# Kernel optimization log

Hardware: AMD Instinct MI355X
Metric: run time of the kernel (lower is better)

## Reference

```python
import jax, jax.numpy as jnp
import numpy as np

N = 4096; E = 32768; H = 128; R = 32; L = 2
CUT_UP = 5.0; MAX_Z = 100

def cosine_cutoff(d):
    c = 0.5 * (jnp.cos(d * (np.pi / CUT_UP)) + 1.0)
    return c * (d < CUT_UP).astype(d.dtype)

def tensor_norm(t):
    return (t * t).sum((-2, -1))

def decompose_tensor(t):
    eye = jnp.eye(3, dtype=t.dtype)
    I = (jnp.trace(t, axis1=-2, axis2=-1) / 3.0)[..., None, None] * eye
    tT = jnp.swapaxes(t, -2, -1)
    A = 0.5 * (t - tT)
    S = 0.5 * (t + tT) - I
    return I, A, S

def vector_to_skewtensor(v):
    x, y, z = v[..., 0], v[..., 1], v[..., 2]
    o = jnp.zeros_like(x)
    return jnp.stack([o, -z, y, z, o, -x, -y, x, o], axis=-1).reshape(v.shape[:-1] + (3, 3))

def vector_to_symtensor(v):
    t = v[..., :, None] * v[..., None, :]
    eye = jnp.eye(3, dtype=v.dtype)
    I = (jnp.trace(t, axis1=-2, axis2=-1) / 3.0)[..., None, None] * eye
    return t - I  # symmetric already, 0.5*(t+t^T) == t

def cmix(T, W):  # nn.Linear(H,H,bias=False) over the channel dim of [N,H,3,3]
    return jnp.einsum('nhij,hk->nkij', T, W)

def layernorm(x, g, b, eps=1e-5):
    m = x.mean(-1, keepdims=True)
    v = ((x - m) ** 2).mean(-1, keepdims=True)
    return (x - m) / jnp.sqrt(v + eps) * g + b

def setup_inputs():
    key = jax.random.key(0)
    ks = iter(jax.random.split(key, 48))
    def nrm(shape, fan_in):
        return jax.random.normal(next(ks), shape, jnp.float32) / np.sqrt(fan_in)
    inp = {}
    inp['z'] = jax.random.randint(next(ks), (N,), 0, MAX_Z)
    inp['edge_index'] = jax.random.randint(next(ks), (2, E), 0, N)
    inp['edge_weight'] = jax.random.uniform(next(ks), (E,), jnp.float32) * CUT_UP
    inp['edge_vec'] = jax.random.normal(next(ks), (E, 3), jnp.float32)
    inp['edge_attr'] = jax.random.normal(next(ks), (E, R), jnp.float32)
    inp['emb_table'] = nrm((MAX_Z, H), H)
    inp['dp1_w'] = nrm((R, H), R); inp['dp1_b'] = jnp.zeros((H,))
    inp['dp2_w'] = nrm((R, H), R); inp['dp2_b'] = jnp.zeros((H,))
    inp['dp3_w'] = nrm((R, H), R); inp['dp3_b'] = jnp.zeros((H,))
    inp['emb2_w'] = nrm((2 * H, H), 2 * H); inp['emb2_b'] = jnp.zeros((H,))
    inp['tne_lt'] = nrm((3, H, H), H)
    inp['tne_s0_w'] = nrm((H, 2 * H), H); inp['tne_s0_b'] = jnp.zeros((2 * H,))
    inp['tne_s1_w'] = nrm((2 * H, 3 * H), 2 * H); inp['tne_s1_b'] = jnp.zeros((3 * H,))
    inp['ln_g'] = jnp.ones((H,)); inp['ln_b'] = jnp.zeros((H,))
    inp['msg_l0_w'] = nrm((L, R, H), R); inp['msg_l0_b'] = jnp.zeros((L, H))
    inp['msg_l1_w'] = nrm((L, H, 2 * H), H); inp['msg_l1_b'] = jnp.zeros((L, 2 * H))
    inp['msg_l2_w'] = nrm((L, 2 * H, 3 * H), 2 * H); inp['msg_l2_b'] = jnp.zeros((L, 3 * H))
    inp['msg_lx'] = nrm((L, 3, H, H), H)
    inp['msg_lt'] = nrm((L, 3, H, H), H)
    return inp

def _forward(z, edge_index, edge_weight, edge_vec, edge_attr, emb_table,
             dp1_w, dp1_b, dp2_w, dp2_b, dp3_w, dp3_b, emb2_w, emb2_b,
             tne_lt, tne_s0_w, tne_s0_b, tne_s1_w, tne_s1_b, ln_g, ln_b,
             msg_l0_w, msg_l0_b, msg_l1_w, msg_l1_b, msg_l2_w, msg_l2_b,
             msg_lx, msg_lt):
    src, dst = edge_index[0], edge_index[1]
    eye = jnp.eye(3, dtype=jnp.float32)
    segsum = lambda x: jax.ops.segment_sum(x, dst, num_segments=N)
    silu = jax.nn.silu
    # ---- TensorNeighborEmbedding ----
    Z = emb_table[z]                                     # [N,H]
    C = cosine_cutoff(edge_weight)                       # [E]
    W1 = (edge_attr @ dp1_w + dp1_b) * C[:, None]
    W2 = (edge_attr @ dp2_w + dp2_b) * C[:, None]
    W3 = (edge_attr @ dp3_w + dp3_b) * C[:, None]
    mask = (src != dst)[:, None]
    vn = jnp.linalg.norm(edge_vec, axis=-1, keepdims=True)
    ev = jnp.where(mask, edge_vec / jnp.maximum(vn, 1e-12), edge_vec)
    skew = vector_to_skewtensor(ev)                      # [E,3,3]
    sym = vector_to_symtensor(ev)                        # [E,3,3]
    Zij = jnp.concatenate([Z[dst], Z[src]], axis=-1) @ emb2_w + emb2_b  # [E,H]
    # I channel is a scaled identity per edge -> factor the eye out of the scatter
    In = segsum(Zij * W1)[..., None, None] * eye                         # [N,H,3,3]
    An = segsum((Zij * W2)[:, :, None, None] * skew[:, None])            # [N,H,3,3]
    Sn = segsum((Zij * W3)[:, :, None, None] * sym[:, None])             # [N,H,3,3]
    norm = layernorm(tensor_norm(In + An + Sn), ln_g, ln_b)              # [N,H]
    In = cmix(In, tne_lt[0]); An = cmix(An, tne_lt[1]); Sn = cmix(Sn, tne_lt[2])
    fsc = silu(silu(norm @ tne_s0_w + tne_s0_b) @ tne_s1_w + tne_s1_b).reshape(N, H, 3)
    X = (fsc[..., 0, None, None] * In + fsc[..., 1, None, None] * An
         + fsc[..., 2, None, None] * Sn)
    # ---- TensorMessage layers ----
    for l in range(L):
        ea = silu(edge_attr @ msg_l0_w[l] + msg_l0_b[l])
        ea = silu(ea @ msg_l1_w[l] + msg_l1_b[l])
        ea = silu(ea @ msg_l2_w[l] + msg_l2_b[l])
        ea = (ea * C[:, None]).reshape(E, H, 3)
        X = X / (tensor_norm(X) + 1.0)[..., None, None]
        I, A, S = decompose_tensor(X)
        I = cmix(I, msg_lx[l, 0]); A = cmix(A, msg_lx[l, 1]); S = cmix(S, msg_lx[l, 2])
        Y = I + A + S
        Im = segsum(ea[:, :, 0, None, None] * I[src])    # gather -> scale -> scatter
        Am = segsum(ea[:, :, 1, None, None] * A[src])
        Sm = segsum(ea[:, :, 2, None, None] * S[src])
        msg = Im + Am + Sm
        AB = msg @ Y + Y @ msg                           # batched 3x3 matmuls
        I, A, S = decompose_tensor(AB)
        d = (tensor_norm(I + A + S) + 1.0)[..., None, None]
        I = cmix(I / d, msg_lt[l, 0]); A = cmix(A / d, msg_lt[l, 1]); S = cmix(S / d, msg_lt[l, 2])
        dX = I + A + S
        dX = dX + dX @ dX
        X = X + dX
    return X

def reference(z, edge_index, edge_weight, edge_vec, edge_attr, emb_table,
              dp1_w, dp1_b, dp2_w, dp2_b, dp3_w, dp3_b, emb2_w, emb2_b,
              tne_lt, tne_s0_w, tne_s0_b, tne_s1_w, tne_s1_b, ln_g, ln_b,
              msg_l0_w, msg_l0_b, msg_l1_w, msg_l1_b, msg_l2_w, msg_l2_b,
              msg_lx, msg_lt):
    return _forward(z, edge_index, edge_weight, edge_vec, edge_attr, emb_table,
                    dp1_w, dp1_b, dp2_w, dp2_b, dp3_w, dp3_b, emb2_w, emb2_b,
                    tne_lt, tne_s0_w, tne_s0_b, tne_s1_w, tne_s1_b, ln_g, ln_b,
                    msg_l0_w, msg_l0_b, msg_l1_w, msg_l1_b, msg_l2_w, msg_l2_b,
                    msg_lx, msg_lt)
```

## Files before the change

### kernel.cpp

```cpp
#include <hip/hip_runtime.h>
#include <hip/hip_bf16.h>

typedef __hip_bfloat16 bf16;
typedef __attribute__((ext_vector_type(8))) short short8v;
typedef __attribute__((ext_vector_type(4))) float f32x4;

#define NN 4096
#define NE 32768
#define HH 128
#define MAXZ 100
#define TPB 8
#define NB 2


__device__ __forceinline__ float b2f(bf16 v){ return __bfloat162float(v); }
__device__ __forceinline__ float ldf(const float* p, size_t i){ return p[i]; }
__device__ __forceinline__ float ldf(const bf16*  p, size_t i){ return __bfloat162float(p[i]); }
__device__ __forceinline__ float siluf(float x){ return x / (1.0f + __expf(-x)); }
__device__ __forceinline__ unsigned short f2bu(float x){
  bf16 h = __float2bfloat16(x);
  return *reinterpret_cast<unsigned short*>(&h);
}

__global__ void __launch_bounds__(256) k_detect(const unsigned int* __restrict__ w, int* __restrict__ flag){
  __shared__ int cnt[256];
  int t = threadIdx.x;
  int c = 0;
  for (int i = t; i < 4096; i += 256){
    unsigned int lo = w[i] & 0xffffu;
    int e = (int)((lo >> 7) & 0xffu);
    c += (e >= 110 && e <= 132) ? 1 : 0;
  }
  cnt[t] = c; __syncthreads();
  for (int off=128; off>=1; off>>=1){ if (t<off) cnt[t]+=cnt[t+off]; __syncthreads(); }
  if (t==0) flag[0] = (cnt[0] < 2048) ? 1 : 0;
}

__global__ void __launch_bounds__(256) k_count(const int* __restrict__ dst, int* __restrict__ counts){
  int e = blockIdx.x*256 + threadIdx.x;
  if (e < NE) atomicAdd(&counts[dst[e]], 1);
}

__global__ void __launch_bounds__(1024) k_scan(const int* __restrict__ counts, int* __restrict__ offsets, int* __restrict__ cursor){
  __shared__ int lds[1024];
  int t = threadIdx.x;
  int c0 = counts[4*t+0], c1 = counts[4*t+1], c2 = counts[4*t+2], c3 = counts[4*t+3];
  int s1 = c0+c1, s2 = s1+c2, s3 = s2+c3;
  lds[t] = s3;
  __syncthreads();
  for (int off=1; off<1024; off<<=1){
    int v = lds[t];
    int add = (t>=off)? lds[t-off] : 0;
    __syncthreads();
    lds[t] = v + add;
    __syncthreads();
  }
  int incl = lds[t];
  int base = incl - s3;
  offsets[4*t+0]=base;    offsets[4*t+1]=base+c0; offsets[4*t+2]=base+s1; offsets[4*t+3]=base+s2;
  cursor [4*t+0]=base;    cursor [4*t+1]=base+c0; cursor [4*t+2]=base+s1; cursor [4*t+3]=base+s2;
  if (t==1023) offsets[4096]=incl;
}

__global__ void __launch_bounds__(256) k_fill(const int* __restrict__ dst, const int* __restrict__ src,
                                              int* __restrict__ cursor,
                                              int* __restrict__ pos, int* __restrict__ csrc){
  int e = blockIdx.x*256 + threadIdx.x;
  if (e < NE){
    int p = atomicAdd(&cursor[dst[e]], 1);
    pos[e] = p;
    csrc[p] = src[e];
  }
}

template<typename T>
__device__ __forceinline__ void geom_impl(const T* ew, const T* evec,
    const int* src, const int* dst, const int* pos, float* gC, float* gVp){
  int e = blockIdx.x*256 + threadIdx.x;
  if (e >= NE) return;
  float d = ldf(ew, e);
  float c = 0.5f*(cosf(d*0.6283185307179586f)+1.0f);
  c = (d < 5.0f) ? c : 0.0f;
  gC[e] = c;
  float x = ldf(evec, (size_t)e*3+0), y = ldf(evec, (size_t)e*3+1), z = ldf(evec, (size_t)e*3+2);
  if (src[e] != dst[e]){
    float n = sqrtf(x*x+y*y+z*z);
    float inv = 1.0f/fmaxf(n, 1e-12f);
    x*=inv; y*=inv; z*=inv;
  }
  int p = pos[e];
  gVp[p*3+0]=x; gVp[p*3+1]=y; gVp[p*3+2]=z;
}
__global__ void __launch_bounds__(256) k_geom(const void* ew, const void* evec,
    const int* __restrict__ src, const int* __restrict__ dst, const int* __restrict__ pos,
    float* __restrict__ gC, float* __restrict__ gVp, const int* __restrict__ flag){
  if (flag[0]) geom_impl<float>((const float*)ew, (const float*)evec, src, dst, pos, gC, gVp);
  else         geom_impl<bf16 >((const bf16* )ew, (const bf16* )evec, src, dst, pos, gC, gVp);
}

template<typename T>
__device__ __forceinline__ void zemb_impl(const T* emb, const T* emb2_w,
    float* P1z, float* P2z, float* Zr){
  int zv = blockIdx.x, h = threadIdx.x;
  Zr[h] = ldf(emb, (size_t)zv*HH + h);
// ... 210 lines not shown
  for (int ks=0; ks<8; ++ks) a3[ks] = *reinterpret_cast<const short8v*>(&h2p[ks*512 + lane*8]);
  for (int nt=wid; nt<24; nt+=4){
    float bias = ldf(b1, nt*16+m);
    f32x4 acc = {bias,bias,bias,bias};
    #pragma unroll
    for (int ks=0; ks<8; ++ks){
      short8v b = *reinterpret_cast<const short8v*>(ps1 + ((size_t)(nt*8+ks)*64 + lane)*8);
      acc = __builtin_amdgcn_mfma_f32_16x16x32_bf16(a3[ks], b, acc, 0,0,0);
    }
    #pragma unroll
    for (int r=0;r<4;++r){
      int n = nt*16 + m, row = g*4 + r;
      ((unsigned short*)fsc3)[(size_t)(n0+row)*384 + (n%3)*128 + (n/3)] = f2bu(siluf(acc[r]));
    }
  }
}
__global__ void __launch_bounds__(256) k_node_mlp(
  const bf16* __restrict__ lnO, const unsigned short* __restrict__ ps0,
  const unsigned short* __restrict__ ps1,
  const void* b0, const void* b1, bf16* __restrict__ fsc3, const int* __restrict__ flag)
{
  __shared__ __align__(16) unsigned short h2p[4096];
  if (flag[0]) node_mlp_impl<float>(lnO, ps0, ps1, (const float*)b0, (const float*)b1, fsc3, h2p);
  else         node_mlp_impl<bf16 >(lnO, ps0, ps1, (const bf16* )b0, (const bf16* )b1, fsc3, h2p);
}

__global__ void __launch_bounds__(256) k_tne_cmix(
  const bf16* __restrict__ sm10, const unsigned short* __restrict__ pwlt,
  const bf16* __restrict__ fsc3, float* __restrict__ X9)
{
  int wid  = threadIdx.x >> 6;
  int lane = threadIdx.x & 63;
  int n0 = blockIdx.x*16;
  int m = lane & 15, g = lane >> 4;
  f32x4 acc[10][2];
  #pragma unroll
  for (int c=0;c<10;++c){ acc[c][0]=(f32x4){0,0,0,0}; acc[c][1]=(f32x4){0,0,0,0}; }
  #pragma unroll
  for (int c=0;c<10;++c){
    int mat = (c==0) ? 0 : (c<4) ? 1 : 2;
    const unsigned short* bw = pwlt + (size_t)mat*16384;
    short8v af[4];
    #pragma unroll
    for (int ks=0; ks<4; ++ks)
      af[ks] = *reinterpret_cast<const short8v*>((const unsigned short*)sm10 + (size_t)(n0+m)*1280 + c*128 + ks*32 + g*8);
    #pragma unroll
    for (int t=0;t<2;++t){
      int nt = wid + t*4;
      #pragma unroll
      for (int ks=0; ks<4; ++ks){
        short8v b = *reinterpret_cast<const short8v*>(bw + ((size_t)(nt*4+ks)*64 + lane)*8);
        acc[c][t] = __builtin_amdgcn_mfma_f32_16x16x32_bf16(af[ks], b, acc[c][t], 0,0,0);
      }
    }
  }
  #pragma unroll
  for (int t=0;t<2;++t){
    int nt = wid + t*4;
    int h = nt*16 + m;
    #pragma unroll
    for (int r=0;r<4;++r){
      int node = n0 + g*4 + r;
      float am  = acc[0][t][r];
      float wm0 = acc[1][t][r], wm1 = acc[2][t][r], wm2 = acc[3][t][r];
      float t0 = acc[4][t][r], t1 = acc[5][t][r], t2 = acc[6][t][r];
      float t3 = acc[7][t][r], t4 = acc[8][t][r], t5 = acc[9][t][r];
      float f0 = b2f(fsc3[(size_t)node*384 + h]);
      float f1 = b2f(fsc3[(size_t)node*384 + 128 + h]);
      float f2 = b2f(fsc3[(size_t)node*384 + 256 + h]);
      float* xp = X9 + (size_t)node*1152;
      xp[0*128+h] = f0*am + f2*t0;
      xp[1*128+h] = -f1*wm2 + f2*t1;
      xp[2*128+h] =  f1*wm1 + f2*t2;
      xp[3*128+h] =  f1*wm2 + f2*t1;
      xp[4*128+h] = f0*am + f2*t3;
      xp[5*128+h] = -f1*wm0 + f2*t4;
      xp[6*128+h] = -f1*wm1 + f2*t2;
      xp[7*128+h] =  f1*wm0 + f2*t4;
      xp[8*128+h] = f0*am + f2*t5;
    }
  }
}

__global__ void __launch_bounds__(256) k_cmix10(
  const bf16* __restrict__ in10, const unsigned short* __restrict__ pw,
  bf16* __restrict__ out10)
{
  int wid  = threadIdx.x >> 6;
  int lane = threadIdx.x & 63;
  int n0 = blockIdx.x*16;
  int m = lane & 15, g = lane >> 4;
  f32x4 acc[10][2];
  #pragma unroll
  for (int c=0;c<10;++c){ acc[c][0]=(f32x4){0,0,0,0}; acc[c][1]=(f32x4){0,0,0,0}; }
  #pragma unroll
  for (int c=0;c<10;++c){
    int mat = (c==0) ? 0 : (c<4) ? 1 : 2;
    const unsigned short* bw = pw + (size_t)mat*16384;
    short8v af[4];
    #pragma unroll
    for (int ks=0; ks<4; ++ks)
      af[ks] = *reinterpret_cast<const short8v*>((const unsigned short*)in10 + (size_t)(n0+m)*1280 + c*128 + ks*32 + g*8);
    #pragma unroll
    for (int t=0;t<2;++t){
      int nt = wid + t*4;
      #pragma unroll
      for (int ks=0; ks<4; ++ks){
        short8v b = *reinterpret_cast<const short8v*>(bw + ((size_t)(nt*4+ks)*64 + lane)*8);
        acc[c][t] = __builtin_amdgcn_mfma_f32_16x16x32_bf16(af[ks], b, acc[c][t], 0,0,0);
      }
    }
  }
  __syncthreads();
  #pragma unroll
  for (int t=0;t<2;++t){
    int nt = wid + t*4;
    int h = nt*16 + m;
    #pragma unroll
    for (int r=0;r<4;++r){
      int node = n0 + g*4 + r;
      unsigned short* op = (unsigned short*)out10 + (size_t)node*1280;
      #pragma unroll
      for (int c=0;c<10;++c) op[c*128 + h] = f2bu(acc[c][t][r]);
    }
  }
}

template<typename T>
__device__ __forceinline__ void mfma_impl(
  const unsigned short* eattr_c, const float* gC, const int* pos,
  const unsigned short* p0, const unsigned short* p1, const unsigned short* p2,
  const T* b0, const T* b1, const T* b2,
  unsigned short* eabuf, unsigned short (*h1p)[2048], unsigned short (*h2p)[4096], int* spos)
{
  int wid  = threadIdx.x >> 6;
  int lane = threadIdx.x & 63;
  int e0 = blockIdx.x*32;
  int m = lane & 15, g = lane >> 4;
  if (threadIdx.x < 32) spos[threadIdx.x] = pos[e0 + threadIdx.x];
  float cc[2][4];
  #pragma unroll
  for (int mt=0;mt<2;++mt)
    #pragma unroll
    for (int r=0;r<4;++r) cc[mt][r] = gC[e0 + mt*16 + g*4 + r];
  short8v a1[2];
  #pragma unroll
  for (int mt=0;mt<2;++mt)
    a1[mt] = *reinterpret_cast<const short8v*>(eattr_c + (size_t)(e0+mt*16+m)*32 + g*8);
  for (int nt=wid; nt<8; nt+=4){
    float bias = ldf(b0, nt*16+m);
    short8v b = *reinterpret_cast<const short8v*>(p0 + ((size_t)nt*64 + lane)*8);
    #pragma unroll
    for (int mt=0;mt<2;++mt){
      f32x4 acc = {bias,bias,bias,bias};
      acc = __builtin_amdgcn_mfma_f32_16x16x32_bf16(a1[mt], b, acc, 0,0,0);
      #pragma unroll
      for (int r=0;r<4;++r){
        int n = nt*16 + m, row = g*4 + r;
        h1p[mt][(n>>5)*512 + (((n>>3)&3)*16+row)*8 + (n&7)] = f2bu(siluf(acc[r]));
      }
    }
  }
  __syncthreads();
  short8v a2[2][4];
  #pragma unroll
  for (int mt=0;mt<2;++mt)
    #pragma unroll
    for (int ks=0; ks<4; ++ks)
      a2[mt][ks] = *reinterpret_cast<const short8v*>(&h1p[mt][ks*512 + lane*8]);
  for (int nt=wid; nt<16; nt+=4){
    float bias = ldf(b1, nt*16+m);
    short8v bfr[4];
    #pragma unroll
    for (int ks=0; ks<4; ++ks)
      bfr[ks] = *reinterpret_cast<const short8v*>(p1 + ((size_t)(nt*4+ks)*64 + lane)*8);
    #pragma unroll
    for (int mt=0;mt<2;++mt){
      f32x4 acc = {bias,bias,bias,bias};
      #pragma unroll
      for (int ks=0; ks<4; ++ks)
        acc = __builtin_amdgcn_mfma_f32_16x16x32_bf16(a2[mt][ks], bfr[ks], acc, 0,0,0);
      #pragma unroll
      for (int r=0;r<4;++r){
        int n = nt*16 + m, row = g*4 + r;
        h2p[mt][(n>>5)*512 + (((n>>3)&3)*16+row)*8 + (n&7)] = f2bu(siluf(acc[r]));
      }
    }
  }
  __syncthreads();
  short8v a3[2][8];
  #pragma unroll
  for (int mt=0;mt<2;++mt)
    #pragma unroll
    for (int ks=0; ks<8; ++ks)
      a3[mt][ks] = *reinterpret_cast<const short8v*>(&h2p[mt][ks*512 + lane*8]);
  for (int nt=wid; nt<24; nt+=4){
    float bias = ldf(b2, nt*16+m);
    short8v bfr[8];
    #pragma unroll
    for (int ks=0; ks<8; ++ks)
      bfr[ks] = *reinterpret_cast<const short8v*>(p2 + ((size_t)(nt*8+ks)*64 + lane)*8);
    #pragma unroll
    for (int mt=0;mt<2;++mt){
      f32x4 acc = {bias,bias,bias,bias};
      #pragma unroll
      for (int ks=0; ks<8; ++ks)
        acc = __builtin_amdgcn_mfma_f32_16x16x32_bf16(a3[mt][ks], bfr[ks], acc, 0,0,0);
      #pragma unroll
      for (int r=0;r<4;++r){
        int n = nt*16 + m, row = g*4 + r;
        float v = siluf(acc[r]) * cc[mt][r];
        eabuf[(size_t)spos[mt*16+row]*384 + (n%3)*128 + (n/3)] = f2bu(v);
      }
    }
  }
}
__global__ void __launch_bounds__(256) k_msg_edge_mfma(
  const unsigned short* __restrict__ eattr_c, const float* __restrict__ gC,
  const int* __restrict__ pos,
  const unsigned short* __restrict__ p0, const unsigned short* __restrict__ p1,
  const unsigned short* __restrict__ p2,
  const void* b0, const void* b1, const void* b2, long boff0, long boff1, long boff2,
  unsigned short* __restrict__ eabuf, const int* __restrict__ flag)
{
  __shared__ __align__(16) unsigned short h1p[2][2048];
  __shared__ __align__(16) unsigned short h2p[2][4096];
  __shared__ int spos[32];
  if (flag[0]) mfma_impl<float>(eattr_c, gC, pos, p0, p1, p2,
      (const float*)b0 + boff0, (const float*)b1 + boff1, (const float*)b2 + boff2, eabuf, h1p, h2p, spos);
  else mfma_impl<bf16>(eattr_c, gC, pos, p0, p1, p2,
      (const bf16*)b0 + boff0, (const bf16*)b1 + boff1, (const bf16*)b2 + boff2, eabuf, h1p, h2p, spos);
}

__global__ void __launch_bounds__(128) k_msg_norm(
  float* __restrict__ X9, bf16* __restrict__ smb)
{
  int n0 = blockIdx.x*NB, h = threadIdx.x;
  #pragma unroll
  for (int nn=0;nn<NB;++nn){
    int n = n0+nn;
    float* xp = X9 + (size_t)n*1152;
    float x00=xp[0*128+h], x01=xp[1*128+h], x02=xp[2*128+h];
    float x10=xp[3*128+h], x11=xp[4*128+h], x12=xp[5*128+h];
    float x20=xp[6*128+h], x21=xp[7*128+h], x22=xp[8*128+h];
    float tn = x00*x00+x01*x01+x02*x02+x10*x10+x11*x11+x12*x12+x20*x20+x21*x21+x22*x22;
    float inv = 1.0f/(tn+1.0f);
    x00*=inv; x01*=inv; x02*=inv; x10*=inv; x11*=inv; x12*=inv; x20*=inv; x21*=inv; x22*=inv;
    xp[0*128+h]=x00; xp[1*128+h]=x01; xp[2*128+h]=x02;
    xp[3*128+h]=x10; xp[4*128+h]=x11; xp[5*128+h]=x12;
    xp[6*128+h]=x20; xp[7*128+h]=x21; xp[8*128+h]=x22;
    float a = (x00+x11+x22)*(1.0f/3.0f);
    bf16* sp = smb + (size_t)n*1280;
    sp[0*128+h]=__float2bfloat16(a);
    sp[1*128+h]=__float2bfloat16(0.5f*(x21-x12));
    sp[2*128+h]=__float2bfloat16(0.5f*(x02-x20));
    sp[3*128+h]=__float2bfloat16(0.5f*(x10-x01));
    sp[4*128+h]=__float2bfloat16(x00-a);
    sp[5*128+h]=__float2bfloat16(0.5f*(x01+x10));
    sp[6*128+h]=__float2bfloat16(0.5f*(x02+x20));
    sp[7*128+h]=__float2bfloat16(x11-a);
    sp[8*128+h]=__float2bfloat16(0.5f*(x12+x21));
    sp[9*128+h]=__float2bfloat16(x22-a);
  }
}

__global__ void __launch_bounds__(128) k_msg_sab(
  const int* __restrict__ offsets, const int* __restrict__ csrc,
  const bf16* __restrict__ eabuf, const bf16* __restrict__ Y10, bf16* __restrict__ smb)
{
  int n0 = blockIdx.x*NB, h = threadIdx.x;
  #pragma unroll
  for (int nn=0;nn<NB;++nn){
    int n = n0+nn;
    float am=0, vm0=0,vm1=0,vm2=0, smm0=0,smm1=0,smm2=0,smm3=0,smm4=0,smm5=0;
    int beg = offsets[n], end = offsets[n+1];
    int i = beg;
    for (; i+4 <= end; i += 4){
      int ss[4];
      #pragma unroll
      for (int u=0;u<4;++u){ ss[u] = csrc[i+u]; }
      float e0a[4], e1a[4], e2a[4];
      float y0[4],y1[4],y2[4],y3[4],y4[4],y5[4],y6[4],y7[4],y8[4],y9[4];
      #pragma unroll
      for (int u=0;u<4;++u){
        const bf16* ep = eabuf + (size_t)(i+u)*384;
        e0a[u]=b2f(ep[h]); e1a[u]=b2f(ep[128+h]); e2a[u]=b2f(ep[256+h]);
        const bf16* yp = Y10 + (size_t)ss[u]*1280;
        y0[u]=b2f(yp[0*128+h]); y1[u]=b2f(yp[1*128+h]); y2[u]=b2f(yp[2*128+h]);
        y3[u]=b2f(yp[3*128+h]); y4[u]=b2f(yp[4*128+h]); y5[u]=b2f(yp[5*128+h]);
        y6[u]=b2f(yp[6*128+h]); y7[u]=b2f(yp[7*128+h]); y8[u]=b2f(yp[8*128+h]);
        y9[u]=b2f(yp[9*128+h]);
      }
      #pragma unroll
      for (int u=0;u<4;++u){
        am   += e0a[u]*y0[u];
        vm0  += e1a[u]*y1[u]; vm1 += e1a[u]*y2[u]; vm2 += e1a[u]*y3[u];
        smm0 += e2a[u]*y4[u]; smm1 += e2a[u]*y5[u]; smm2 += e2a[u]*y6[u];
        smm3 += e2a[u]*y7[u]; smm4 += e2a[u]*y8[u]; smm5 += e2a[u]*y9[u];
      }
    }
    for (; i<end; ++i){
      int s = csrc[i];
      const bf16* ep = eabuf + (size_t)i*384;
      float e0 = b2f(ep[h]), e1 = b2f(ep[128+h]), e2 = b2f(ep[256+h]);
      const bf16* yp = Y10 + (size_t)s*1280;
      am   += e0*b2f(yp[0*128+h]);
      vm0  += e1*b2f(yp[1*128+h]); vm1 += e1*b2f(yp[2*128+h]); vm2 += e1*b2f(yp[3*128+h]);
      smm0 += e2*b2f(yp[4*128+h]); smm1 += e2*b2f(yp[5*128+h]); smm2 += e2*b2f(yp[6*128+h]);
      smm3 += e2*b2f(yp[7*128+h]); smm4 += e2*b2f(yp[8*128+h]); smm5 += e2*b2f(yp[9*128+h]);
    }
    const bf16* yp = Y10 + (size_t)n*1280;
    float aY=b2f(yp[0*128+h]), u0=b2f(yp[1*128+h]), u1=b2f(yp[2*128+h]), u2=b2f(yp[3*128+h]);
    float q0=b2f(yp[4*128+h]), q1=b2f(yp[5*128+h]), q2=b2f(yp[6*128+h]);
    float q3=b2f(yp[7*128+h]), q4=b2f(yp[8*128+h]), q5=b2f(yp[9*128+h]);
    float m00=am+smm0,   m01=-vm2+smm1, m02= vm1+smm2;
    float m10= vm2+smm1, m11=am+smm3,  m12=-vm0+smm4;
    float m20=-vm1+smm2, m21= vm0+smm4, m22=am+smm5;
    float y00=aY+q0,  y01=-u2+q1, y02= u1+q2;
    float y10= u2+q1, y11=aY+q3,  y12=-u0+q4;
    float y20=-u1+q2, y21= u0+q4, y22=aY+q5;
    float ab00 = m00*y00+m01*y10+m02*y20 + y00*m00+y01*m10+y02*m20;
    float ab01 = m00*y01+m01*y11+m02*y21 + y00*m01+y01*m11+y02*m21;
    float ab02 = m00*y02+m01*y12+m02*y22 + y00*m02+y01*m12+y02*m22;
    float ab10 = m10*y00+m11*y10+m12*y20 + y10*m00+y11*m10+y12*m20;
    float ab11 = m10*y01+m11*y11+m12*y21 + y10*m01+y11*m11+y12*m21;
    float ab12 = m10*y02+m11*y12+m12*y22 + y10*m02+y11*m12+y12*m22;
    float ab20 = m20*y00+m21*y10+m22*y20 + y20*m00+y21*m10+y22*m20;
    float ab21 = m20*y01+m21*y11+m22*y21 + y20*m01+y21*m11+y22*m21;
    float ab22 = m20*y02+m21*y12+m22*y22 + y20*m02+y21*m12+y22*m22;
    float a2 = (ab00+ab11+ab22)*(1.0f/3.0f);
    float w0 = 0.5f*(ab21-ab12), w1 = 0.5f*(ab02-ab20), w2 = 0.5f*(ab10-ab01);
    float t0 = ab00-a2, t1 = 0.5f*(ab01+ab10), t2 = 0.5f*(ab02+ab20);
    float t3 = ab11-a2, t4 = 0.5f*(ab12+ab21), t5 = ab22-a2;
    float dnm = ab00*ab00+ab01*ab01+ab02*ab02+ab10*ab10+ab11*ab11+ab12*ab12
              + ab20*ab20+ab21*ab21+ab22*ab22 + 1.0f;
    float inv = 1.0f/dnm;
    bf16* sp = smb + (size_t)n*1280;
    sp[0*128+h]=__float2bfloat16(a2*inv);
    sp[1*128+h]=__float2bfloat16(w0*inv); sp[2*128+h]=__float2bfloat16(w1*inv); sp[3*128+h]=__float2bfloat16(w2*inv);
    sp[4*128+h]=__float2bfloat16(t0*inv); sp[5*128+h]=__float2bfloat16(t1*inv); sp[6*128+h]=__float2bfloat16(t2*inv);
    sp[7*128+h]=__float2bfloat16(t3*inv); sp[8*128+h]=__float2bfloat16(t4*inv); sp[9*128+h]=__float2bfloat16(t5*inv);
  }
}

template<typename T>
__device__ __forceinline__ void fin_impl(
  const bf16* smb, float* X9, T* out, int write_out)
{
  int n0 = blockIdx.x*NB, h = threadIdx.x;
  #pragma unroll
  for (int nn=0;nn<NB;++nn){
    int n = n0+nn;
    const bf16* sp = smb + (size_t)n*1280;
    float at  = b2f(sp[0*128+h]);
    float vt0 = b2f(sp[1*128+h]), vt1 = b2f(sp[2*128+h]), vt2 = b2f(sp[3*128+h]);
    float st0 = b2f(sp[4*128+h]), st1 = b2f(sp[5*128+h]), st2 = b2f(sp[6*128+h]);
    float st3 = b2f(sp[7*128+h]), st4 = b2f(sp[8*128+h]), st5 = b2f(sp[9*128+h]);
    float d00=at+st0,   d01=-vt2+st1, d02= vt1+st2;
    float d10= vt2+st1, d11=at+st3,  d12=-vt0+st4;
    float d20=-vt1+st2, d21= vt0+st4, d22=at+st5;
    float g00 = d00 + d00*d00+d01*d10+d02*d20;
    float g01 = d01 + d00*d01+d01*d11+d02*d21;
    float g02 = d02 + d00*d02+d01*d12+d02*d22;
    float g10 = d10 + d10*d00+d11*d10+d12*d20;
    float g11 = d11 + d10*d01+d11*d11+d12*d21;
    float g12 = d12 + d10*d02+d11*d12+d12*d22;
    float g20 = d20 + d20*d00+d21*d10+d22*d20;
    float g21 = d21 + d20*d01+d21*d11+d22*d21;
    float g22 = d22 + d20*d02+d21*d12+d22*d22;
    float* xp = X9 + (size_t)n*1152;
    float x00=xp[0*128+h]+g00, x01=xp[1*128+h]+g01, x02=xp[2*128+h]+g02;
    float x10=xp[3*128+h]+g10, x11=xp[4*128+h]+g11, x12=xp[5*128+h]+g12;
    float x20=xp[6*128+h]+g20, x21=xp[7*128+h]+g21, x22=xp[8*128+h]+g22;
    if (write_out){
      if (sizeof(T)==4){
        float* of = (float*)out + ((size_t)n*128 + h)*9;
        of[0]=x00; of[1]=x01; of[2]=x02; of[3]=x10; of[4]=x11; of[5]=x12; of[6]=x20; of[7]=x21; of[8]=x22;
      } else {
        bf16* ob = (bf16*)out + ((size_t)n*128 + h)*9;
        ob[0]=__float2bfloat16(x00); ob[1]=__float2bfloat16(x01); ob[2]=__float2bfloat16(x02);
        ob[3]=__float2bfloat16(x10); ob[4]=__float2bfloat16(x11); ob[5]=__float2bfloat16(x12);
        ob[6]=__float2bfloat16(x20); ob[7]=__float2bfloat16(x21); ob[8]=__float2bfloat16(x22);
      }
    } else {
      xp[0*128+h]=x00; xp[1*128+h]=x01; xp[2*128+h]=x02;
      xp[3*128+h]=x10; xp[4*128+h]=x11; xp[5*128+h]=x12;
      xp[6*128+h]=x20; xp[7*128+h]=x21; xp[8*128+h]=x22;
    }
  }
}
__global__ void __launch_bounds__(128) k_msg_fin(
  const bf16* __restrict__ smb, float* __restrict__ X9, void* __restrict__ out,
  const int* __restrict__ flag, int write_out)
{
  if (flag[0]) fin_impl<float>(smb, X9, (float*)out, write_out);
  else         fin_impl<bf16 >(smb, X9, (bf16* )out, write_out);
}

extern "C" void kernel_launch(void* const* d_in, const int* in_sizes, int n_in,
                              void* d_out, int out_size, void* d_ws, size_t ws_size,
                              hipStream_t stream)
{
  (void)in_sizes; (void)n_in; (void)out_size; (void)ws_size;
  const int* z    = (const int*)d_in[0];
  const int* eidx = (const int*)d_in[1];
  const int* src  = eidx;
  const int* dst  = eidx + NE;

  char* w = (char*)d_ws;
  int* flag    = (int*)w;   w += 64;
  int* counts  = (int*)w;   w += (size_t)NN*4;
  int* offsets = (int*)w;   w += (size_t)(NN+1)*4 + 60;
  int* cursor  = (int*)w;   w += (size_t)NN*4;
  int* pos     = (int*)w;   w += (size_t)NE*4;
  int* csrc    = (int*)w;   w += (size_t)NE*4;
  float* gC    = (float*)w; w += (size_t)NE*4;
  float* gVp   = (float*)w; w += (size_t)NE*12;
  float* P1z   = (float*)w; w += (size_t)MAXZ*HH*4;
  float* P2z   = (float*)w; w += (size_t)MAXZ*HH*4;
  bf16* eabuf  = (bf16*)w;  w += (size_t)NE*384*2;
  float* X9    = (float*)w; w += (size_t)NN*1152*4;
  bf16* Y10    = (bf16*)w;  w += (size_t)NN*1280*2;
  bf16* smb    = (bf16*)w;  w += (size_t)NN*1280*2;
  unsigned short* eattr_c = (unsigned short*)w; w += (size_t)NE*32*2;
  unsigned short* pw0[2]; unsigned short* pw1[2]; unsigned short* pw2[2];
  for (int l=0;l<2;++l){
    pw0[l] = (unsigned short*)w; w += 8*64*8*2;
    pw1[l] = (unsigned short*)w; w += 64*64*8*2;
    pw2[l] = (unsigned short*)w; w += 192*64*8*2;
  }
  unsigned short* pw_s0 = (unsigned short*)w; w += 64*64*8*2;
  unsigned short* pw_s1 = (unsigned short*)w; w += 192*64*8*2;
  unsigned short* pwlt  = (unsigned short*)w; w += 3*32*64*8*2;
  unsigned short* pwlx2 = (unsigned short*)w; w += 2*3*32*64*8*2;
  unsigned short* pwlt2 = (unsigned short*)w; w += 2*3*32*64*8*2;
  bf16* lnO    = (bf16*)w;  w += (size_t)NN*128*2;
  bf16* fsc3   = (bf16*)w;  w += (size_t)NN*384*2;
  bf16* sm10   = Y10;

  k_detect<<<1, 256, 0, stream>>>((const unsigned int*)d_in[4], flag);
  hipMemsetAsync(counts, 0, (size_t)NN*4, stream);
  k_count<<<NE/256, 256, 0, stream>>>(dst, counts);
  k_scan<<<1, 1024, 0, stream>>>(counts, offsets, cursor);
  k_fill<<<NE/256, 256, 0, stream>>>(dst, src, cursor, pos, csrc);
  k_geom<<<NE/256, 256, 0, stream>>>(d_in[2], d_in[3], src, dst, pos, gC, gVp, flag);
  k_zemb<<<MAXZ, 128, 0, stream>>>(d_in[5], d_in[12], P1z, P2z, flag);
  k_cvt_attr<<<NE*32/256, 256, 0, stream>>>(d_in[4], eattr_c, flag);

  PackDescs pd;
  for (int l=0;l<2;++l){
    pd.base[l*3+0] = d_in[21]; pd.eoff[l*3+0] = (long)l*32*128;
    pd.base[l*3+1] = d_in[23]; pd.eoff[l*3+1] = (long)l*128*256;
    pd.base[l*3+2] = d_in[25]; pd.eoff[l*3+2] = (long)l*256*384;
    pd.out[l*3+0] = pw0[l]; pd.K[l*3+0]=32;  pd.N[l*3+0]=128;
    pd.out[l*3+1] = pw1[l]; pd.K[l*3+1]=128; pd.N[l*3+1]=256;
    pd.out[l*3+2] = pw2[l]; pd.K[l*3+2]=256; pd.N[l*3+2]=384;
  }
  pd.base[6] = d_in[15]; pd.eoff[6] = 0; pd.out[6] = pw_s0; pd.K[6]=128; pd.N[6]=256;
  pd.base[7] = d_in[17]; pd.eoff[7] = 0; pd.out[7] = pw_s1; pd.K[7]=256; pd.N[7]=384;
  for (int c=0;c<3;++c){
    pd.base[8+c] = d_in[14]; pd.eoff[8+c] = (long)c*16384;
    pd.out[8+c] = pwlt + (size_t)c*16384; pd.K[8+c]=128; pd.N[8+c]=128;
  }
  for (int l=0;l<2;++l)
    for (int c=0;c<3;++c){
      pd.base[11+l*3+c] = d_in[27]; pd.eoff[11+l*3+c] = (long)(l*3+c)*16384;
      pd.out[11+l*3+c] = pwlx2 + (size_t)(l*3+c)*16384; pd.K[11+l*3+c]=128; pd.N[11+l*3+c]=128;
      pd.base[17+l*3+c] = d_in[28]; pd.eoff[17+l*3+c] = (long)(l*3+c)*16384;
      pd.out[17+l*3+c] = pwlt2 + (size_t)(l*3+c)*16384; pd.K[17+l*3+c]=128; pd.N[17+l*3+c]=128;
    }
  k_pack<<<dim3(48, 23), 256, 0, stream>>>(pd, flag);

  k_tne_edge<<<NE/TPB, 128, 0, stream>>>(d_in[4], src, dst, z, pos,
      d_in[6], d_in[7], d_in[8], d_in[9], d_in[10], d_in[11], d_in[13],
      P1z, P2z, gC, eabuf, flag);
  k_tne_scat<<<NN/NB, 128, 0, stream>>>(offsets, gVp, eabuf,
      d_in[19], d_in[20], sm10, lnO, flag);
  k_node_mlp<<<NN/16, 256, 0, stream>>>(lnO, pw_s0, pw_s1, d_in[16], d_in[18], fsc3, flag);
  k_tne_cmix<<<NN/16, 256, 0, stream>>>(sm10, pwlt, fsc3, X9);

  for (int l=0; l<2; ++l){
    k_msg_edge_mfma<<<NE/32, 256, 0, stream>>>(eattr_c, gC, pos, pw0[l], pw1[l], pw2[l],
        d_in[22], d_in[24], d_in[26], (long)l*128, (long)l*256, (long)l*384,
        (unsigned short*)eabuf, flag);
    k_msg_norm<<<NN/NB, 128, 0, stream>>>(X9, smb);
    k_cmix10<<<NN/16, 256, 0, stream>>>(smb, pwlx2 + (size_t)l*3*16384, Y10);
    k_msg_sab<<<NN/NB, 128, 0, stream>>>(offsets, csrc, eabuf, Y10, smb);
    k_cmix10<<<NN/16, 256, 0, stream>>>(smb, pwlt2 + (size_t)l*3*16384, smb);
    k_msg_fin<<<NN/NB, 128, 0, stream>>>(smb, X9, d_out, flag, (l==1)?1:0);
  }
}
```

Before: 279.9 us.

## Fuse node norm into cmix and cmix into final update kernel

Merges the per-node normalize/decompose step into the first channel-mix MFMA kernel, staging the bf16 components in shared memory instead of a global buffer. It also fuses the second channel-mix with the final dX + dX@dX update, consuming the MFMA accumulators directly (rounded to bf16 to match prior numerics). This cuts two kernel launches per layer and the global round trips through smb, at the cost of a 40KB shared buffer per block and fewer blocks for the elementwise work.

```diff
diff --git a/kernel.cpp b/kernel.cpp
--- a/kernel.cpp
+++ b/kernel.cpp
@@ -20,6 +20,10 @@
 __device__ __forceinline__ unsigned short f2bu(float x){
   bf16 h = __float2bfloat16(x);
   return *reinterpret_cast<unsigned short*>(&h);
+}
+__device__ __forceinline__ float bround(float x){
+  bf16 h = __float2bfloat16(x);
+  return __bfloat162float(h);
 }
 
 __global__ void __launch_bounds__(256) k_detect(const unsigned int* __restrict__ w, int* __restrict__ flag){
@@ -396,164 +400,17 @@
   }
 }
 
-__global__ void __launch_bounds__(256) k_cmix10(
-  const bf16* __restrict__ in10, const unsigned short* __restrict__ pw,
-  bf16* __restrict__ out10)
-{
-  int wid  = threadIdx.x >> 6;
-  int lane = threadIdx.x & 63;
+__global__ void __launch_bounds__(256) k_cmix_norm(
+  float* __restrict__ X9, const unsigned short* __restrict__ pw, bf16* __restrict__ Y10)
+{
+  __shared__ __align__(16) unsigned short sst[16*1280];
   int n0 = blockIdx.x*16;
-  int m = lane & 15, g = lane >> 4;
-  f32x4 acc[10][2];
-  #pragma unroll
-  for (int c=0;c<10;++c){ acc[c][0]=(f32x4){0,0,0,0}; acc[c][1]=(f32x4){0,0,0,0}; }
-  #pragma unroll
-  for (int c=0;c<10;++c){
-    int mat = (c==0) ? 0 : (c<4) ? 1 : 2;
-    const unsigned short* bw = pw + (size_t)mat*16384;
-    short8v af[4];
-    #pragma unroll
-    for (int ks=0; ks<4; ++ks)
-      af[ks] = *reinterpret_cast<const short8v*>((const unsigned short*)in10 + (size_t)(n0+m)*1280 + c*128 + ks*32 + g*8);
-    #pragma unroll
-    for (int t=0;t<2;++t){
-      int nt = wid + t*4;
-      #pragma unroll
-      for (int ks=0; ks<4; ++ks){
-        short8v b = *reinterpret_cast<const short8v*>(bw + ((size_t)(nt*4+ks)*64 + lane)*8);
-        acc[c][t] = __builtin_amdgcn_mfma_f32_16x16x32_bf16(af[ks], b, acc[c][t], 0,0,0);
-      }
-    }
-  }
-  __syncthreads();
-  #pragma unroll
-  for (int t=0;t<2;++t){
-    int nt = wid + t*4;
-    int h = nt*16 + m;
-    #pragma unroll
-    for (int r=0;r<4;++r){
-      int node = n0 + g*4 + r;
-      unsigned short* op = (unsigned short*)out10 + (size_t)node*1280;
-      #pragma unroll
-      for (int c=0;c<10;++c) op[c*128 + h] = f2bu(acc[c][t][r]);
-    }
-  }
-}
-
-template<typename T>
-__device__ __forceinline__ void mfma_impl(
-  const unsigned short* eattr_c, const float* gC, const int* pos,
-  const unsigned short* p0, const unsigned short* p1, const unsigned short* p2,
-  const T* b0, const T* b1, const T* b2,
-  unsigned short* eabuf, unsigned short (*h1p)[2048], unsigned short (*h2p)[4096], int* spos)
-{
-  int wid  = threadIdx.x >> 6;
-  int lane = threadIdx.x & 63;
-  int e0 = blockIdx.x*32;
-  int m = lane & 15, g = lane >> 4;
-  if (threadIdx.x < 32) spos[threadIdx.x] = pos[e0 + threadIdx.x];
-  float cc[2][4];
-  #pragma unroll
-  for (int mt=0;mt<2;++mt)
-    #pragma unroll
-    for (int r=0;r<4;++r) cc[mt][r] = gC[e0 + mt*16 + g*4 + r];
-  short8v a1[2];
-  #pragma unroll
-  for (int mt=0;mt<2;++mt)
-    a1[mt] = *reinterpret_cast<const short8v*>(eattr_c + (size_t)(e0+mt*16+m)*32 + g*8);
-  for (int nt=wid; nt<8; nt+=4){
-    float bias = ldf(b0, nt*16+m);
-    short8v b = *reinterpret_cast<const short8v*>(p0 + ((size_t)nt*64 + lane)*8);
-    #pragma unroll
-    for (int mt=0;mt<2;++mt){
-      f32x4 acc = {bias,bias,bias,bias};
-      acc = __builtin_amdgcn_mfma_f32_16x16x32_bf16(a1[mt], b, acc, 0,0,0);
-      #pragma unroll
-      for (int r=0;r<4;++r){
-        int n = nt*16 + m, row = g*4 + r;
-        h1p[mt][(n>>5)*512 + (((n>>3)&3)*16+row)*8 + (n&7)] = f2bu(siluf(acc[r]));
-      }
-    }
-  }
-  __syncthreads();
-  short8v a2[2][4];
-  #pragma unroll
-  for (int mt=0;mt<2;++mt)
-    #pragma unroll
-    for (int ks=0; ks<4; ++ks)
-      a2[mt][ks] = *reinterpret_cast<const short8v*>(&h1p[mt][ks*512 + lane*8]);
-  for (int nt=wid; nt<16; nt+=4){
-    float bias = ldf(b1, nt*16+m);
-    short8v bfr[4];
-    #pragma unroll
-    for (int ks=0; ks<4; ++ks)
-      bfr[ks] = *reinterpret_cast<const short8v*>(p1 + ((size_t)(nt*4+ks)*64 + lane)*8);
-    #pragma unroll
-    for (int mt=0;mt<2;++mt){
-      f32x4 acc = {bias,bias,bias,bias};
-      #pragma unroll
-      for (int ks=0; ks<4; ++ks)
-        acc = __builtin_amdgcn_mfma_f32_16x16x32_bf16(a2[mt][ks], bfr[ks], acc, 0,0,0);
-      #pragma unroll
-      for (int r=0;r<4;++r){
-        int n = nt*16 + m, row = g*4 + r;
-        h2p[mt][(n>>5)*512 + (((n>>3)&3)*16+row)*8 + (n&7)] = f2bu(siluf(acc[r]));
-      }
-    }
-  }
-  __syncthreads();
-  short8v a3[2][8];
-  #pragma unroll
-  for (int mt=0;mt<2;++mt)
-    #pragma unroll
-    for (int ks=0; ks<8; ++ks)
-      a3[mt][ks] = *reinterpret_cast<const short8v*>(&h2p[mt][ks*512 + lane*8]);
-  for (int nt=wid; nt<24; nt+=4){
-    float bias = ldf(b2, nt*16+m);
-    short8v bfr[8];
-    #pragma unroll
-    for (int ks=0; ks<8; ++ks)
-      bfr[ks] = *reinterpret_cast<const short8v*>(p2 + ((size_t)(nt*8+ks)*64 + lane)*8);
-    #pragma unroll
-    for (int mt=0;mt<2;++mt){
-      f32x4 acc = {bias,bias,bias,bias};
-      #pragma unroll
-      for (int ks=0; ks<8; ++ks)
-        acc = __builtin_amdgcn_mfma_f32_16x16x32_bf16(a3[mt][ks], bfr[ks], acc, 0,0,0);
-      #pragma unroll
-      for (int r=0;r<4;++r){
-        int n = nt*16 + m, row = g*4 + r;
-        float v = siluf(acc[r]) * cc[mt][r];
-        eabuf[(size_t)spos[mt*16+row]*384 + (n%3)*128 + (n/3)] = f2bu(v);
-      }
-    }
-  }
-}
-__global__ void __launch_bounds__(256) k_msg_edge_mfma(
-  const unsigned short* __restrict__ eattr_c, const float* __restrict__ gC,
-  const int* __restrict__ pos,
-  const unsigned short* __restrict__ p0, const unsigned short* __restrict__ p1,
-  const unsigned short* __restrict__ p2,
-  const void* b0, const void* b1, const void* b2, long boff0, long boff1, long boff2,
-  unsigned short* __restrict__ eabuf, const int* __restrict__ flag)
-{
-  __shared__ __align__(16) unsigned short h1p[2][2048];
-  __shared__ __align__(16) unsigned short h2p[2][4096];
-  __shared__ int spos[32];
-  if (flag[0]) mfma_impl<float>(eattr_c, gC, pos, p0, p1, p2,
-      (const float*)b0 + boff0, (const float*)b1 + boff1, (const float*)b2 + boff2, eabuf, h1p, h2p, spos);
-  else mfma_impl<bf16>(eattr_c, gC, pos, p0, p1, p2,
-      (const bf16*)b0 + boff0, (const bf16*)b1 + boff1, (const bf16*)b2 + boff2, eabuf, h1p, h2p, spos);
-}
-
-__global__ void __launch_bounds__(128) k_msg_norm(
-  float* __restrict__ X9, bf16* __restrict__ smb)
-{
-  int n0 = blockIdx.x*NB, h = threadIdx.x;
-  #pragma unroll
-  for (int nn=0;nn<NB;++nn){
-    int n = n0+nn;
-    float* xp = X9 + (size_t)n*1152;
+  int tid = threadIdx.x;
+  #pragma unroll
+  for (int it=0; it<8; ++it){
+    int idx = it*256 + tid;
+    int nn = idx >> 7, h = idx & 127;
+    float* xp = X9 + (size_t)(n0+nn)*1152;
     float x00=xp[0*128+h], x01=xp[1*128+h], x02=xp[2*128+h];
     float x10=xp[3*128+h], x11=xp[4*128+h], x12=xp[5*128+h];
     float x20=xp[6*128+h], x21=xp[7*128+h], x22=xp[8*128+h];
@@ -564,18 +421,161 @@
     xp[3*128+h]=x10; xp[4*128+h]=x11; xp[5*128+h]=x12;
     xp[6*128+h]=x20; xp[7*128+h]=x21; xp[8*128+h]=x22;
     float a = (x00+x11+x22)*(1.0f/3.0f);
-    bf16* sp = smb + (size_t)n*1280;
-    sp[0*128+h]=__float2bfloat16(a);
-    sp[1*128+h]=__float2bfloat16(0.5f*(x21-x12));
-    sp[2*128+h]=__float2bfloat16(0.5f*(x02-x20));
-    sp[3*128+h]=__float2bfloat16(0.5f*(x10-x01));
-    sp[4*128+h]=__float2bfloat16(x00-a);
-    sp[5*128+h]=__float2bfloat16(0.5f*(x01+x10));
-    sp[6*128+h]=__float2bfloat16(0.5f*(x02+x20));
-    sp[7*128+h]=__float2bfloat16(x11-a);
-    sp[8*128+h]=__float2bfloat16(0.5f*(x12+x21));
-    sp[9*128+h]=__float2bfloat16(x22-a);
-  }
+    unsigned short* sp = sst + (size_t)nn*1280;
+    sp[0*128+h]=f2bu(a);
+    sp[1*128+h]=f2bu(0.5f*(x21-x12));
+    sp[2*128+h]=f2bu(0.5f*(x02-x20));
+    sp[3*128+h]=f2bu(0.5f*(x10-x01));
+    sp[4*128+h]=f2bu(x00-a);
+    sp[5*128+h]=f2bu(0.5f*(x01+x10));
+    sp[6*128+h]=f2bu(0.5f*(x02+x20));
+    sp[7*128+h]=f2bu(x11-a);
+    sp[8*128+h]=f2bu(0.5f*(x12+x21));
+    sp[9*128+h]=f2bu(x22-a);
+  }
+  __syncthreads();
+  int wid  = tid >> 6;
+  int lane = tid & 63;
+  int m = lane & 15, g = lane >> 4;
+  f32x4 acc[10][2];
+  #pragma unroll
+  for (int c=0;c<10;++c){ acc[c][0]=(f32x4){0,0,0,0}; acc[c][1]=(f32x4){0,0,0,0}; }
+  #pragma unroll
+  for (int c=0;c<10;++c){
+    int mat = (c==0) ? 0 : (c<4) ? 1 : 2;
+    const unsigned short* bw = pw + (size_t)mat*16384;
+    short8v af[4];
+    #pragma unroll
+    for (int ks=0; ks<4; ++ks)
+      af[ks] = *reinterpret_cast<const short8v*>(&sst[(size_t)m*1280 + c*128 + ks*32 + g*8]);
+    #pragma unroll
+    for (int t=0;t<2;++t){
+      int nt = wid + t*4;
+      #pragma unroll
+      for (int ks=0; ks<4; ++ks){
+        short8v b = *reinterpret_cast<const short8v*>(bw + ((size_t)(nt*4+ks)*64 + lane)*8);
+        acc[c][t] = __builtin_amdgcn_mfma_f32_16x16x32_bf16(af[ks], b, acc[c][t], 0,0,0);
+      }
+    }
+  }
+  #pragma unroll
+  for (int t=0;t<2;++t){
+    int nt = wid + t*4;
+    int h = nt*16 + m;
+    #pragma unroll
+    for (int r=0;r<4;++r){
+      int node = n0 + g*4 + r;
+      unsigned short* op = (unsigned short*)Y10 + (size_t)node*1280;
+      #pragma unroll
+      for (int c=0;c<10;++c) op[c*128 + h] = f2bu(acc[c][t][r]);
+    }
+  }
+}
+
+template<typename T>
+__device__ __forceinline__ void mfma_impl(
+  const unsigned short* eattr_c, const float* gC, const int* pos,
+  const unsigned short* p0, const unsigned short* p1, const unsigned short* p2,
+  const T* b0, const T* b1, const T* b2,
+  unsigned short* eabuf, unsigned short (*h1p)[2048], unsigned short (*h2p)[4096], int* spos)
+{
+  int wid  = threadIdx.x >> 6;
+  int lane = threadIdx.x & 63;
+  int e0 = blockIdx.x*32;
+  int m = lane & 15, g = lane >> 4;
+  if (threadIdx.x < 32) spos[threadIdx.x] = pos[e0 + threadIdx.x];
+  float cc[2][4];
+  #pragma unroll
+  for (int mt=0;mt<2;++mt)
+    #pragma unroll
+    for (int r=0;r<4;++r) cc[mt][r] = gC[e0 + mt*16 + g*4 + r];
+  short8v a1[2];
+  #pragma unroll
+  for (int mt=0;mt<2;++mt)
+    a1[mt] = *reinterpret_cast<const short8v*>(eattr_c + (size_t)(e0+mt*16+m)*32 + g*8);
+  for (int nt=wid; nt<8; nt+=4){
+    float bias = ldf(b0, nt*16+m);
+    short8v b = *reinterpret_cast<const short8v*>(p0 + ((size_t)nt*64 + lane)*8);
+    #pragma unroll
+    for (int mt=0;mt<2;++mt){
+      f32x4 acc = {bias,bias,bias,bias};
+      acc = __builtin_amdgcn_mfma_f32_16x16x32_bf16(a1[mt], b, acc, 0,0,0);
+      #pragma unroll
+      for (int r=0;r<4;++r){
+        int n = nt*16 + m, row = g*4 + r;
+        h1p[mt][(n>>5)*512 + (((n>>3)&3)*16+row)*8 + (n&7)] = f2bu(siluf(acc[r]));
+      }
+    }
+  }
+  __syncthreads();
+  short8v a2[2][4];
+  #pragma unroll
+  for (int mt=0;mt<2;++mt)
+    #pragma unroll
+    for (int ks=0; ks<4; ++ks)
+      a2[mt][ks] = *reinterpret_cast<const short8v*>(&h1p[mt][ks*512 + lane*8]);
+  for (int nt=wid; nt<16; nt+=4){
+    float bias = ldf(b1, nt*16+m);
+    short8v bfr[4];
+    #pragma unroll
+    for (int ks=0; ks<4; ++ks)
+      bfr[ks] = *reinterpret_cast<const short8v*>(p1 + ((size_t)(nt*4+ks)*64 + lane)*8);
+    #pragma unroll
+    for (int mt=0;mt<2;++mt){
+      f32x4 acc = {bias,bias,bias,bias};
+      #pragma unroll
+      for (int ks=0; ks<4; ++ks)
+        acc = __builtin_amdgcn_mfma_f32_16x16x32_bf16(a2[mt][ks], bfr[ks], acc, 0,0,0);
+      #pragma unroll
+      for (int r=0;r<4;++r){
+        int n = nt*16 + m, row = g*4 + r;
+        h2p[mt][(n>>5)*512 + (((n>>3)&3)*16+row)*8 + (n&7)] = f2bu(siluf(acc[r]));
+      }
+    }
+  }
+  __syncthreads();
+  short8v a3[2][8];
+  #pragma unroll
+  for (int mt=0;mt<2;++mt)
+    #pragma unroll
+    for (int ks=0; ks<8; ++ks)
+      a3[mt][ks] = *reinterpret_cast<const short8v*>(&h2p[mt][ks*512 + lane*8]);
+  for (int nt=wid; nt<24; nt+=4){
+    float bias = ldf(b2, nt*16+m);
+    short8v bfr[8];
+    #pragma unroll
+    for (int ks=0; ks<8; ++ks)
+      bfr[ks] = *reinterpret_cast<const short8v*>(p2 + ((size_t)(nt*8+ks)*64 + lane)*8);
+    #pragma unroll
+    for (int mt=0;mt<2;++mt){
+      f32x4 acc = {bias,bias,bias,bias};
+      #pragma unroll
+      for (int ks=0; ks<8; ++ks)
+        acc = __builtin_amdgcn_mfma_f32_16x16x32_bf16(a3[mt][ks], bfr[ks], acc, 0,0,0);
+      #pragma unroll
+      for (int r=0;r<4;++r){
+        int n = nt*16 + m, row = g*4 + r;
+        float v = siluf(acc[r]) * cc[mt][r];
+        eabuf[(size_t)spos[mt*16+row]*384 + (n%3)*128 + (n/3)] = f2bu(v);
+      }
+    }
+  }
+}
+__global__ void __launch_bounds__(256) k_msg_edge_mfma(
+  const unsigned short* __restrict__ eattr_c, const float* __restrict__ gC,
+  const int* __restrict__ pos,
+  const unsigned short* __restrict__ p0, const unsigned short* __restrict__ p1,
+  const unsigned short* __restrict__ p2,
+  const void* b0, const void* b1, const void* b2, long boff0, long boff1, long boff2,
+  unsigned short* __restrict__ eabuf, const int* __restrict__ flag)
+{
+  __shared__ __align__(16) unsigned short h1p[2][2048];
+  __shared__ __align__(16) unsigned short h2p[2][4096];
+  __shared__ int spos[32];
+  if (flag[0]) mfma_impl<float>(eattr_c, gC, pos, p0, p1, p2,
+      (const float*)b0 + boff0, (const float*)b1 + boff1, (const float*)b2 + boff2, eabuf, h1p, h2p, spos);
+  else mfma_impl<bf16>(eattr_c, gC, pos, p0, p1, p2,
+      (const bf16*)b0 + boff0, (const bf16*)b1 + boff1, (const bf16*)b2 + boff2, eabuf, h1p, h2p, spos);
 }
 
 __global__ void __launch_bounds__(128) k_msg_sab(
@@ -658,57 +658,86 @@
 }
 
 template<typename T>
-__device__ __forceinline__ void fin_impl(
-  const bf16* smb, float* X9, T* out, int write_out)
-{
-  int n0 = blockIdx.x*NB, h = threadIdx.x;
-  #pragma unroll
-  for (int nn=0;nn<NB;++nn){
-    int n = n0+nn;
-    const bf16* sp = smb + (size_t)n*1280;
-    float at  = b2f(sp[0*128+h]);
-    float vt0 = b2f(sp[1*128+h]), vt1 = b2f(sp[2*128+h]), vt2 = b2f(sp[3*128+h]);
-    float st0 = b2f(sp[4*128+h]), st1 = b2f(sp[5*128+h]), st2 = b2f(sp[6*128+h]);
-    float st3 = b2f(sp[7*128+h]), st4 = b2f(sp[8*128+h]), st5 = b2f(sp[9*128+h]);
-    float d00=at+st0,   d01=-vt2+st1, d02= vt1+st2;
-    float d10= vt2+st1, d11=at+st3,  d12=-vt0+st4;
-    float d20=-vt1+st2, d21= vt0+st4, d22=at+st5;
-    float g00 = d00 + d00*d00+d01*d10+d02*d20;
-    float g01 = d01 + d00*d01+d01*d11+d02*d21;
-    float g02 = d02 + d00*d02+d01*d12+d02*d22;
-    float g10 = d10 + d10*d00+d11*d10+d12*d20;
-    float g11 = d11 + d10*d01+d11*d11+d12*d21;
-    float g12 = d12 + d10*d02+d11*d12+d12*d22;
-    float g20 = d20 + d20*d00+d21*d10+d22*d20;
-    float g21 = d21 + d20*d01+d21*d11+d22*d21;
-    float g22 = d22 + d20*d02+d21*d12+d22*d22;
-    float* xp = X9 + (size_t)n*1152;
-    float x00=xp[0*128+h]+g00, x01=xp[1*128+h]+g01, x02=xp[2*128+h]+g02;
-    float x10=xp[3*128+h]+g10, x11=xp[4*128+h]+g11, x12=xp[5*128+h]+g12;
-    float x20=xp[6*128+h]+g20, x21=xp[7*128+h]+g21, x22=xp[8*128+h]+g22;
-    if (write_out){
-      if (sizeof(T)==4){
-        float* of = (float*)out + ((size_t)n*128 + h)*9;
-        of[0]=x00; of[1]=x01; of[2]=x02; of[3]=x10; of[4]=x11; of[5]=x12; of[6]=x20; of[7]=x21; of[8]=x22;
+__device__ __forceinline__ void cmix_fin_impl(
+  const bf16* smb, const unsigned short* pw, float* X9, T* out, int write_out)
+{
+  int wid  = threadIdx.x >> 6;
+  int lane = threadIdx.x & 63;
+  int n0 = blockIdx.x*16;
+  int m = lane & 15, g = lane >> 4;
+  f32x4 acc[10][2];
+  #pragma unroll
+  for (int c=0;c<10;++c){ acc[c][0]=(f32x4){0,0,0,0}; acc[c][1]=(f32x4){0,0,0,0}; }
+  #pragma unroll
+  for (int c=0;c<10;++c){
+    int mat = (c==0) ? 0 : (c<4) ? 1 : 2;
+    const unsigned short* bw = pw + (size_t)mat*16384;
+    short8v af[4];
+    #pragma unroll
+    for (int ks=0; ks<4; ++ks)
+      af[ks] = *reinterpret_cast<const short8v*>((const unsigned short*)smb + (size_t)(n0+m)*1280 + c*128 + ks*32 + g*8);
+    #pragma unroll
+    for (int t=0;t<2;++t){
+      int nt = wid + t*4;
+      #pragma unroll
+      for (int ks=0; ks<4; ++ks){
+        short8v b = *reinterpret_cast<const short8v*>(bw + ((size_t)(nt*4+ks)*64 + lane)*8);
+        acc[c][t] = __builtin_amdgcn_mfma_f32_16x16x32_bf16(af[ks], b, acc[c][t], 0,0,0);
+      }
+    }
+  }
+  #pragma unroll
+  for (int t=0;t<2;++t){
+    int nt = wid + t*4;
+    int h = nt*16 + m;
+    #pragma unroll
+    for (int r=0;r<4;++r){
+      int node = n0 + g*4 + r;
+      float at  = bround(acc[0][t][r]);
+      float vt0 = bround(acc[1][t][r]), vt1 = bround(acc[2][t][r]), vt2 = bround(acc[3][t][r]);
+      float st0 = bround(acc[4][t][r]), st1 = bround(acc[5][t][r]), st2 = bround(acc[6][t][r]);
+      float st3 = bround(acc[7][t][r]), st4 = bround(acc[8][t][r]), st5 = bround(acc[9][t][r]);
+      float d00=at+st0,   d01=-vt2+st1, d02= vt1+st2;
+      float d10= vt2+st1, d11=at+st3,  d12=-vt0+st4;
+      float d20=-vt1+st2, d21= vt0+st4, d22=at+st5;
+      float g00 = d00 + d00*d00+d01*d10+d02*d20;
+      float g01 = d01 + d00*d01+d01*d11+d02*d21;
+      float g02 = d02 + d00*d02+d01*d12+d02*d22;
+      float g10 = d10 + d10*d00+d11*d10+d12*d20;
+      float g11 = d11 + d10*d01+d11*d11+d12*d21;
+      float g12 = d12 + d10*d02+d11*d12+d12*d22;
+      float g20 = d20 + d20*d00+d21*d10+d22*d20;
+      float g21 = d21 + d20*d01+d21*d11+d22*d21;
+      float g22 = d22 + d20*d02+d21*d12+d22*d22;
+      float* xp = X9 + (size_t)node*1152;
+      float x00=xp[0*128+h]+g00, x01=xp[1*128+h]+g01, x02=xp[2*128+h]+g02;
+      float x10=xp[3*128+h]+g10, x11=xp[4*128+h]+g11, x12=xp[5*128+h]+g12;
+      float x20=xp[6*128+h]+g20, x21=xp[7*128+h]+g21, x22=xp[8*128+h]+g22;
+      if (write_out){
+        if (sizeof(T)==4){
+          float* of = (float*)out + ((size_t)node*128 + h)*9;
+          of[0]=x00; of[1]=x01; of[2]=x02; of[3]=x10; of[4]=x11; of[5]=x12; of[6]=x20; of[7]=x21; of[8]=x22;
+        } else {
+          bf16* ob = (bf16*)out + ((size_t)node*128 + h)*9;
+          ob[0]=__float2bfloat16(x00); ob[1]=__float2bfloat16(x01); ob[2]=__float2bfloat16(x02);
+          ob[3]=__float2bfloat16(x10); ob[4]=__float2bfloat16(x11); ob[5]=__float2bfloat16(x12);
+          ob[6]=__float2bfloat16(x20); ob[7]=__float2bfloat16(x21); ob[8]=__float2bfloat16(x22);
+        }
       } else {
-        bf16* ob = (bf16*)out + ((size_t)n*128 + h)*9;
-        ob[0]=__float2bfloat16(x00); ob[1]=__float2bfloat16(x01); ob[2]=__float2bfloat16(x02);
-        ob[3]=__float2bfloat16(x10); ob[4]=__float2bfloat16(x11); ob[5]=__float2bfloat16(x12);
-        ob[6]=__float2bfloat16(x20); ob[7]=__float2bfloat16(x21); ob[8]=__float2bfloat16(x22);
-      }
-    } else {
-      xp[0*128+h]=x00; xp[1*128+h]=x01; xp[2*128+h]=x02;
-      xp[3*128+h]=x10; xp[4*128+h]=x11; xp[5*128+h]=x12;
-      xp[6*128+h]=x20; xp[7*128+h]=x21; xp[8*128+h]=x22;
-    }
-  }
-}
-__global__ void __launch_bounds__(128) k_msg_fin(
-  const bf16* __restrict__ smb, float* __restrict__ X9, void* __restrict__ out,
+        xp[0*128+h]=x00; xp[1*128+h]=x01; xp[2*128+h]=x02;
+        xp[3*128+h]=x10; xp[4*128+h]=x11; xp[5*128+h]=x12;
+        xp[6*128+h]=x20; xp[7*128+h]=x21; xp[8*128+h]=x22;
+      }
+    }
+  }
+}
+__global__ void __launch_bounds__(256) k_cmix_fin(
+  const bf16* __restrict__ smb, const unsigned short* __restrict__ pw,
+  float* __restrict__ X9, void* __restrict__ out,
   const int* __restrict__ flag, int write_out)
 {
-  if (flag[0]) fin_impl<float>(smb, X9, (float*)out, write_out);
-  else         fin_impl<bf16 >(smb, X9, (bf16* )out, write_out);
+  if (flag[0]) cmix_fin_impl<float>(smb, pw, X9, (float*)out, write_out);
+  else         cmix_fin_impl<bf16 >(smb, pw, X9, (bf16* )out, write_out);
 }
 
 extern "C" void kernel_launch(void* const* d_in, const int* in_sizes, int n_in,
@@ -797,10 +826,9 @@
     k_msg_edge_mfma<<<NE/32, 256, 0, stream>>>(eattr_c, gC, pos, pw0[l], pw1[l], pw2[l],
         d_in[22], d_in[24], d_in[26], (long)l*128, (long)l*256, (long)l*384,
         (unsigned short*)eabuf, flag);
-    k_msg_norm<<<NN/NB, 128, 0, stream>>>(X9, smb);
-    k_cmix10<<<NN/16, 256, 0, stream>>>(smb, pwlx2 + (size_t)l*3*16384, Y10);
+    k_cmix_norm<<<NN/16, 256, 0, stream>>>(X9, pwlx2 + (size_t)l*3*16384, Y10);
     k_msg_sab<<<NN/NB, 128, 0, stream>>>(offsets, csrc, eabuf, Y10, smb);
-    k_cmix10<<<NN/16, 256, 0, stream>>>(smb, pwlt2 + (size_t)l*3*16384, smb);
-    k_msg_fin<<<NN/NB, 128, 0, stream>>>(smb, X9, d_out, flag, (l==1)?1:0);
-  }
-}
+    k_cmix_fin<<<NN/16, 256, 0, stream>>>(smb, pwlt2 + (size_t)l*3*16384, X9, d_out,
+        flag, (l==1)?1:0);
+  }
+}
```

After: 261.5 us. -6.5%, faster.
